# Optimization experiments

Hardware: AMD Instinct MI355X
Metric: run time of the kernel (lower is better)

Reference implementation:

```python
import jax, jax.numpy as jnp
import numpy as np

N_NODES = 2000
NEG_SLOPE = 0.01  # torch nn.LeakyReLU default


def setup_inputs() -> dict:
    key = jax.random.key(0)
    ks = jax.random.split(key, 7)
    B, T, N, F, E = 4, 12, N_NODES, 64, 32000
    state = jax.random.normal(ks[0], (B, T, N, F), dtype=jnp.float32)
    feature = jax.random.normal(ks[1], (N, F), dtype=jnp.float32)
    W = jax.random.normal(ks[2], (F, 2 * F), dtype=jnp.float32) / np.sqrt(2 * F)
    b = jnp.zeros((F,), dtype=jnp.float32)
    src = jax.random.randint(ks[3], (E,), 0, N)
    dst = jax.random.randint(ks[4], (E,), 0, N)
    dist = jax.random.uniform(ks[5], (E, 1), dtype=jnp.float32)
    return {"state": state, "feature": feature, "W": W, "b": b,
            "src": src, "dst": dst, "dist": dist}


def reference(state, feature, W, b, src, dst, dist):
    # state: [B,T,N,F] -> node-major [N,B,T,F] (matches unsqueeze/transpose/squeeze)
    s = jnp.moveaxis(state, 2, 0)                       # [N,B,T,F]
    s_src = s[src]                                      # [E,B,T,F] gather
    s_dst = s[dst]                                      # [E,B,T,F]
    h = jnp.concatenate([s_src, s_dst], axis=-1)        # [E,B,T,2F]
    alpha = jnp.einsum('ebtk,fk->ebtf', h, W) + b       # linear 2F->F
    alpha = jnp.where(alpha >= 0, alpha, NEG_SLOPE * alpha)  # LeakyReLU
    alpha = alpha * dist[:, None, None, :]              # dist [E,1] broadcast
    # segment softmax over incoming edges per destination node
    n = s.shape[0]
    m = jax.ops.segment_max(alpha, dst, num_segments=n)        # [N,B,T,F]
    ex = jnp.exp(alpha - m[dst])
    denom = jax.ops.segment_sum(ex, dst, num_segments=n)       # [N,B,T,F]
    w = ex / denom[dst]                                         # [E,B,T,F]
    new_state = jax.ops.segment_sum(w * s_src, dst, num_segments=n)
    new_state = jax.nn.relu(new_state)                  # [N,B,T,F]
    return jnp.moveaxis(new_state, 0, 2)                # [B,T,N,F]
```

## Files before the change

kernel.cpp:

```cpp
#include <hip/hip_runtime.h>
#include <hip/hip_bf16.h>
#include <hip/hip_fp16.h>
#include <math.h>


#define F_DIM 64
#define LOG2E 1.442695040888963f
#define CPAD 128
#define RSTRIDE 128

typedef _Float16 f16x8 __attribute__((ext_vector_type(8)));
typedef float f32x4 __attribute__((ext_vector_type(4)));


__global__ void hist_kernel(const int* __restrict__ dst, int* __restrict__ chunk_hist,
                            int E, int N) {
    __shared__ int h[2048];
    int t = threadIdx.x, c = blockIdx.x;
    for (int i = t; i < N; i += 256) h[i] = 0;
    __syncthreads();
    int e = c * 256 + t;
    if (e < E) atomicAdd(&h[dst[e]], 1);
    __syncthreads();
    for (int d = t; d < N; d += 256)
        chunk_hist[d * CPAD + c] = h[d];
}

__global__ void binscan_kernel(int* __restrict__ chunk_hist, int* __restrict__ counts,
                               int* __restrict__ esrc, float* __restrict__ edist,
                               int N, int C) {
    int wave = (blockIdx.x * blockDim.x + threadIdx.x) >> 6;
    int lane = threadIdx.x & 63;
    if (wave >= N) return;
    int* row = chunk_hist + wave * CPAD;
    int i0 = 2 * lane, i1 = 2 * lane + 1;
    int v0 = (i0 < C) ? row[i0] : 0;
    int v1 = (i1 < C) ? row[i1] : 0;
    int s = v0 + v1;
    int acc = s;
#pragma unroll
    for (int d = 1; d < 64; d <<= 1) {
        int up = __shfl_up(acc, d);
        if (lane >= d) acc += up;
    }
    int excl = acc - s;
    if (i0 < C) row[i0] = excl;
    if (i1 < C) row[i1] = excl + v0;
    int total = __shfl(acc, 63);
    if (lane == 63) counts[wave] = total;
    int padend = (total + 7) & ~7;
    if (padend > RSTRIDE) padend = RSTRIDE;
    int* er = esrc + wave * RSTRIDE;
    float* dr = edist + wave * RSTRIDE;
    if (i0 >= total && i0 < padend) { er[i0] = 0; dr[i0] = 0.f; }
    if (i1 >= total && i1 < padend) { er[i1] = 0; dr[i1] = 0.f; }
}

__global__ void scatter2_kernel(const int* __restrict__ dst, const int* __restrict__ src,
                                const float* __restrict__ dist,
                                const int* __restrict__ chunk_hist,
                                int* __restrict__ esrc, float* __restrict__ edist, int E) {
    __shared__ int sdst[256];
    int t = threadIdx.x, c = blockIdx.x;
    int e = c * 256 + t;
    int d = (e < E) ? dst[e] : -1;
    sdst[t] = d;
    __syncthreads();
    if (e >= E) return;
    int cnt = 0;
#pragma unroll 8
    for (int j = 0; j < 256; j++)
        cnt += (j < t && sdst[j] == d) ? 1 : 0;
    int off = chunk_hist[d * CPAD + c] + cnt;
    if (off < RSTRIDE) {
        esrc[d * RSTRIDE + off] = src[e] << 8;
        edist[d * RSTRIDE + off] = dist[e] * LOG2E;
    }
}

__global__ __launch_bounds__(256) void gemm_pre_mfma(
    const float* __restrict__ state, const float* __restrict__ W,
    const float* __restrict__ bias,
    unsigned* __restrict__ PSh, float* __restrict__ P2B) {
    int tid = threadIdx.x;
    int wv = tid >> 6, lane = tid & 63;
    int l15 = lane & 15, l4 = lane >> 4;

    f16x8 bf[8][2];
#pragma unroll
    for (int ct = 0; ct < 8; ++ct) {
        int j = ct * 16 + l15;
        const float* wp = (j < 64) ? (W + j * 128) : (W + (j - 64) * 128 + 64);
#pragma unroll
        for (int kh = 0; kh < 2; ++kh) {
            const float* p = wp + kh * 32 + l4 * 8;
            float4 w0 = *(const float4*)p;
            float4 w1 = *(const float4*)(p + 4);
            f16x8 h;
            h[0] = (_Float16)w0.x; h[1] = (_Float16)w0.y;
            h[2] = (_Float16)w0.z; h[3] = (_Float16)w0.w;
            h[4] = (_Float16)w1.x; h[5] = (_Float16)w1.y;
            h[6] = (_Float16)w1.z; h[7] = (_Float16)w1.w;
            bf[ct][kh] = h;
        }
    }
    float b0 = bias[l15], b1 = bias[16 + l15], b2 = bias[32 + l15], b3 = bias[48 + l15];

    int r = blockIdx.x * 64 + wv * 16;

    const float* ap = state + (long)(r + l15) * 64 + l4 * 8;
    float4 a0 = *(const float4*)ap;
    float4 a1 = *(const float4*)(ap + 4);
    float4 a2 = *(const float4*)(ap + 32);
    float4 a3 = *(const float4*)(ap + 36);
    f16x8 af0, af1;
    af0[0] = (_Float16)a0.x; af0[1] = (_Float16)a0.y;
    af0[2] = (_Float16)a0.z; af0[3] = (_Float16)a0.w;
    af0[4] = (_Float16)a1.x; af0[5] = (_Float16)a1.y;
    af0[6] = (_Float16)a1.z; af0[7] = (_Float16)a1.w;
    af1[0] = (_Float16)a2.x; af1[1] = (_Float16)a2.y;
    af1[2] = (_Float16)a2.z; af1[3] = (_Float16)a2.w;
    af1[4] = (_Float16)a3.x; af1[5] = (_Float16)a3.y;
    af1[6] = (_Float16)a3.z; af1[7] = (_Float16)a3.w;

    f32x4 zero = {0.f, 0.f, 0.f, 0.f};
    f32x4 acc[8];
#pragma unroll
    for (int ct = 0; ct < 8; ++ct) {
        acc[ct] = __builtin_amdgcn_mfma_f32_16x16x32_f16(af0, bf[ct][0], zero, 0, 0, 0);
        acc[ct] = __builtin_amdgcn_mfma_f32_16x16x32_f16(af1, bf[ct][1], acc[ct], 0, 0, 0);
    }

    float bb0[4] = {b0, b1, b2, b3};
#pragma unroll
    for (int reg = 0; reg < 4; ++reg) {
        long rr = r + l4 * 4 + reg;
        const float* sp = state + rr * 64;
#pragma unroll
        for (int ct = 0; ct < 4; ++ct) {
            float sval = sp[ct * 16 + l15];
            __half2 h = __floats2half2_rn(acc[ct][reg], sval);
            PSh[rr * 64 + ct * 16 + l15] = *(unsigned*)&h;
        }
#pragma unroll
        for (int ct = 4; ct < 8; ++ct) {
            P2B[rr * 64 + (ct - 4) * 16 + l15] = acc[ct][reg] + bb0[ct - 4];
        }
    }
}


#define ECOMP(U, D, DEN, NUM)                                 \
    {                                                         \
        float2 ps = __half22float2(*(const __half2*)&(U));    \
        float x = ps.x + p2;                                  \
        x = fmaxf(x, 0.01f * x);                              \
        x *= (D);                                             \
        float p = __builtin_amdgcn_exp2f(x);                  \
        DEN += p;                                             \
        NUM = fmaf(p, ps.y, NUM);                             \
    }

#define G8(A, B, a0, a1, a2, a3, a4, a5, a6, a7)              \
    unsigned a0 = *(const unsigned*)(PSb + (A).x + f4);       \
    unsigned a1 = *(const unsigned*)(PSb + (A).y + f4);       \
    unsigned a2 = *(const unsigned*)(PSb + (A).z + f4);       \
    unsigned a3 = *(const unsigned*)(PSb + (A).w + f4);       \
    unsigned a4 = *(const unsigned*)(PSb + (B).x + f4);       \
    unsigned a5 = *(const unsigned*)(PSb + (B).y + f4);       \
    unsigned a6 = *(const unsigned*)(PSb + (B).z + f4);       \
    unsigned a7 = *(const unsigned*)(PSb + (B).w + f4);

#define E8(DA, DB, a0, a1, a2, a3, a4, a5, a6, a7)            \
    ECOMP(a0, (DA).x, den0, num0)                             \
    ECOMP(a1, (DA).y, den1, num1)                             \
    ECOMP(a2, (DA).z, den0, num0)                             \
    ECOMP(a3, (DA).w, den1, num1)                             \
    ECOMP(a4, (DB).x, den0, num0)                             \
    ECOMP(a5, (DB).y, den1, num1)                             \
    ECOMP(a6, (DB).z, den0, num0)                             \
    ECOMP(a7, (DB).w, den1, num1)

__global__ __launch_bounds__(384) void gat_kernel(
    const unsigned* __restrict__ PSh, const float* __restrict__ P2B,
    const int* __restrict__ esrc, const float* __restrict__ edist,
    const int* __restrict__ counts,
    float* __restrict__ out, int N, int NBT) {
    int b = blockIdx.x;
    int xcd = b & 7, n = b >> 3;
    int w = threadIdx.x >> 6, f = threadIdx.x & 63;
    int bt = xcd * 6 + w;
    const char* PSb = (const char*)PSh + (size_t)bt * N * 256;
    int f4 = f << 2;
    int obase = ((bt * N + n) << 6) + f;
    float p2 = P2B[obase];
    int cnt = counts[n];
    const int4*   ep4 = (const int4*)(esrc + n * RSTRIDE);
    const float4* dp4 = (const float4*)(edist + n * RSTRIDE);
    float o = 0.f;
    if (cnt > 0) {
        unsigned z = *(const unsigned*)(PSb + f4);
        float2 zf = __half22float2(*(const __half2*)&z);
        float den0 = 0.f, den1 = 0.f, num0 = 0.f, num1 = 0.f;
        int cm = (cnt > RSTRIDE) ? RSTRIDE : cnt;
        int nq = (cm + 7) >> 3;
        for (int q = 0; q < nq; ++q) {
            int4   sa = ep4[2 * q], sb = ep4[2 * q + 1];
            float4 da = dp4[2 * q], db = dp4[2 * q + 1];
            G8(sa, sb, v0, v1, v2, v3, v4, v5, v6, v7)
            E8(da, db, v0, v1, v2, v3, v4, v5, v6, v7)
        }
        float npad = (float)((nq << 3) - cm);
        o = fmaxf((num0 + num1 - npad * zf.y) / (den0 + den1 - npad), 0.f);
    }
    out[obase] = o;
}


extern "C" void kernel_launch(void* const* d_in, const int* in_sizes, int n_in,
                              void* d_out, int out_size, void* d_ws, size_t ws_size,
                              hipStream_t stream) {
    const float* state = (const float*)d_in[0];
    const float* W     = (const float*)d_in[2];
    const float* bias  = (const float*)d_in[3];
    const int*   src   = (const int*)d_in[4];
    const int*   dst   = (const int*)d_in[5];
    const float* dist  = (const float*)d_in[6];
    float* out = (float*)d_out;

    int N   = in_sizes[1] / F_DIM;
    int E   = in_sizes[4];
    int NBT = in_sizes[0] / (N * F_DIM);
    int C   = (E + 255) / 256;

    size_t pelems = (size_t)NBT * N * F_DIM;
    unsigned* PSh = (unsigned*)d_ws;
    float* P2B = (float*)(PSh + pelems);
    int* counts     = (int*)(P2B + pelems);
    int* chunk_hist = counts + 2048;
    int* esrc       = chunk_hist + N * CPAD;
    float* edist    = (float*)(esrc + N * RSTRIDE);

    hist_kernel<<<C, 256, 0, stream>>>(dst, chunk_hist, E, N);
    binscan_kernel<<<(N * 64 + 255) / 256, 256, 0, stream>>>(chunk_hist, counts,
                                                             esrc, edist, N, C);
    scatter2_kernel<<<C, 256, 0, stream>>>(dst, src, dist, chunk_hist, esrc, edist, E);

    int total_rows = NBT * N;
    gemm_pre_mfma<<<total_rows / 64, 256, 0, stream>>>(state, W, bias, PSh, P2B);

    gat_kernel<<<N * 8, 384, 0, stream>>>(PSh, P2B, esrc, edist, counts, out, N, NBT);
}
```

Measured before the change: 92.02 us.

## Pad edge lists to 4, fuse fp16 converts via fma_mix, two nodes per block

Each destination node's edge list is now padded to a multiple of 4 instead of 8, so fewer dummy edges are gathered and exponentiated. The gather loop moves into a helper that processes 4 edges per iteration. It uses inline v_fma_mix_f32 to read the fp16 packed values directly, with no separate half-to-float conversion. LeakyReLU is applied after scaling by dist, which is equivalent only because dist is non-negative. Each block now handles two nodes, halving the grid and sharing setup loads, but this assumes N is even and gives less memory-level parallelism per loop iteration.

```diff
diff --git a/kernel.cpp b/kernel.cpp
--- a/kernel.cpp
+++ b/kernel.cpp
@@ -48,7 +48,7 @@
     if (i1 < C) row[i1] = excl + v0;
     int total = __shfl(acc, 63);
     if (lane == 63) counts[wave] = total;
-    int padend = (total + 7) & ~7;
+    int padend = (total + 3) & ~3;
     if (padend > RSTRIDE) padend = RSTRIDE;
     int* er = esrc + wave * RSTRIDE;
     float* dr = edist + wave * RSTRIDE;
@@ -150,36 +150,42 @@
 }
 
 
-#define ECOMP(U, D, DEN, NUM)                                 \
-    {                                                         \
-        float2 ps = __half22float2(*(const __half2*)&(U));    \
-        float x = ps.x + p2;                                  \
-        x = fmaxf(x, 0.01f * x);                              \
-        x *= (D);                                             \
-        float p = __builtin_amdgcn_exp2f(x);                  \
-        DEN += p;                                             \
-        NUM = fmaf(p, ps.y, NUM);                             \
-    }
-
-#define G8(A, B, a0, a1, a2, a3, a4, a5, a6, a7)              \
-    unsigned a0 = *(const unsigned*)(PSb + (A).x + f4);       \
-    unsigned a1 = *(const unsigned*)(PSb + (A).y + f4);       \
-    unsigned a2 = *(const unsigned*)(PSb + (A).z + f4);       \
-    unsigned a3 = *(const unsigned*)(PSb + (A).w + f4);       \
-    unsigned a4 = *(const unsigned*)(PSb + (B).x + f4);       \
-    unsigned a5 = *(const unsigned*)(PSb + (B).y + f4);       \
-    unsigned a6 = *(const unsigned*)(PSb + (B).z + f4);       \
-    unsigned a7 = *(const unsigned*)(PSb + (B).w + f4);
-
-#define E8(DA, DB, a0, a1, a2, a3, a4, a5, a6, a7)            \
-    ECOMP(a0, (DA).x, den0, num0)                             \
-    ECOMP(a1, (DA).y, den1, num1)                             \
-    ECOMP(a2, (DA).z, den0, num0)                             \
-    ECOMP(a3, (DA).w, den1, num1)                             \
-    ECOMP(a4, (DB).x, den0, num0)                             \
-    ECOMP(a5, (DB).y, den1, num1)                             \
-    ECOMP(a6, (DB).z, den0, num0)                             \
-    ECOMP(a7, (DB).w, den1, num1)
+#define ECOMP(U, D, P2V, DEN, NUM)                                        \
+    {                                                                     \
+        float x;                                                          \
+        asm("v_fma_mix_f32 %0, %1, %2, %3 op_sel:[0,0,0] op_sel_hi:[1,0,0]" \
+            : "=v"(x) : "v"(U), "v"(fone), "v"(P2V));                     \
+        float y0 = x * (D);                                               \
+        float y1 = 0.01f * y0;                                            \
+        float y = fmaxf(y0, y1);                                          \
+        float p = __builtin_amdgcn_exp2f(y);                              \
+        DEN += p;                                                         \
+        asm("v_fma_mix_f32 %0, %1, %2, %0 op_sel:[0,1,0] op_sel_hi:[0,1,0]" \
+            : "+v"(NUM) : "v"(p), "v"(U));                                \
+    }
+
+__device__ __forceinline__ float gat_node(
+    int cnt, const int4* __restrict__ ep4, const float4* __restrict__ dp4,
+    float p2v, const char* PSb, int f4, float fone, float zs) {
+    if (cnt <= 0) return 0.f;
+    float den0 = 0.f, den1 = 0.f, num0 = 0.f, num1 = 0.f;
+    int cm = (cnt > RSTRIDE) ? RSTRIDE : cnt;
+    int nq = (cm + 3) >> 2;
+    for (int q = 0; q < nq; ++q) {
+        int4   sa = ep4[q];
+        float4 da = dp4[q];
+        unsigned a0 = *(const unsigned*)(PSb + sa.x + f4);
+        unsigned a1 = *(const unsigned*)(PSb + sa.y + f4);
+        unsigned a2 = *(const unsigned*)(PSb + sa.z + f4);
+        unsigned a3 = *(const unsigned*)(PSb + sa.w + f4);
+        ECOMP(a0, da.x, p2v, den0, num0)
+        ECOMP(a1, da.y, p2v, den1, num1)
+        ECOMP(a2, da.z, p2v, den0, num0)
+        ECOMP(a3, da.w, p2v, den1, num1)
+    }
+    float npad = (float)((nq << 2) - cm);
+    return fmaxf((num0 + num1 - npad * zs) / (den0 + den1 - npad), 0.f);
+}
 
 __global__ __launch_bounds__(384) void gat_kernel(
     const unsigned* __restrict__ PSh, const float* __restrict__ P2B,
@@ -187,33 +193,26 @@
     const int* __restrict__ counts,
     float* __restrict__ out, int N, int NBT) {
     int b = blockIdx.x;
-    int xcd = b & 7, n = b >> 3;
+    int xcd = b & 7, pr = b >> 3;
     int w = threadIdx.x >> 6, f = threadIdx.x & 63;
     int bt = xcd * 6 + w;
     const char* PSb = (const char*)PSh + (size_t)bt * N * 256;
     int f4 = f << 2;
-    int obase = ((bt * N + n) << 6) + f;
-    float p2 = P2B[obase];
-    int cnt = counts[n];
-    const int4*   ep4 = (const int4*)(esrc + n * RSTRIDE);
-    const float4* dp4 = (const float4*)(edist + n * RSTRIDE);
-    float o = 0.f;
-    if (cnt > 0) {
-        unsigned z = *(const unsigned*)(PSb + f4);
-        float2 zf = __half22float2(*(const __half2*)&z);
-        float den0 = 0.f, den1 = 0.f, num0 = 0.f, num1 = 0.f;
-        int cm = (cnt > RSTRIDE) ? RSTRIDE : cnt;
-        int nq = (cm + 7) >> 3;
-        for (int q = 0; q < nq; ++q) {
-            int4   sa = ep4[2 * q], sb = ep4[2 * q + 1];
-            float4 da = dp4[2 * q], db = dp4[2 * q + 1];
-            G8(sa, sb, v0, v1, v2, v3, v4, v5, v6, v7)
-            E8(da, db, v0, v1, v2, v3, v4, v5, v6, v7)
-        }
-        float npad = (float)((nq << 3) - cm);
-        o = fmaxf((num0 + num1 - npad * zf.y) / (den0 + den1 - npad), 0.f);
-    }
-    out[obase] = o;
+    int n0 = pr * 2, n1 = n0 + 1;
+    int cnt0 = counts[n0], cnt1 = counts[n1];
+    const int4*   ep0 = (const int4*)(esrc + n0 * RSTRIDE);
+    const float4* dp0 = (const float4*)(edist + n0 * RSTRIDE);
+    const int4*   ep1 = (const int4*)(esrc + n1 * RSTRIDE);
+    const float4* dp1 = (const float4*)(edist + n1 * RSTRIDE);
+    int ob0 = ((bt * N + n0) << 6) + f;
+    int ob1 = ob0 + 64;
+    float p2_0 = P2B[ob0];
+    float p2_1 = P2B[ob1];
+    unsigned z = *(const unsigned*)(PSb + f4);
+    float zs = __half22float2(*(const __half2*)&z).y;
+    float fone = 1.0f;
+    out[ob0] = gat_node(cnt0, ep0, dp0, p2_0, PSb, f4, fone, zs);
+    out[ob1] = gat_node(cnt1, ep1, dp1, p2_1, PSb, f4, fone, zs);
 }
 
 
@@ -249,5 +248,6 @@
     int total_rows = NBT * N;
     gemm_pre_mfma<<<total_rows / 64, 256, 0, stream>>>(state, W, bias, PSh, P2B);
 
-    gat_kernel<<<N * 8, 384, 0, stream>>>(PSh, P2B, esrc, edist, counts, out, N, NBT);
-}
+    gat_kernel<<<(N / 2) * 8, 384, 0, stream>>>(PSh, P2B, esrc, edist, counts,
+                                                out, N, NBT);
+}
```

New measurement: 93.04 us. No clear change (+1.1%).
